# Kernel tuning notes

Hardware: AMD Instinct MI355X
Metric: run time of the kernel (lower is better)

Reference implementation:

```python
import jax, jax.numpy as jnp
import numpy as np

B, DIM, MID, H, W = 4, 256, 128, 128, 128
EPS = 1e-5


def _conv(x, w, pad):
    # x: [B,C,H,W], w: [O,I,k,k]
    return jax.lax.conv_general_dilated(
        x, w, window_strides=(1, 1), padding=[(pad, pad), (pad, pad)],
        dimension_numbers=('NCHW', 'OIHW', 'NCHW'))


def _bn(x, g, b, m, v):
    inv = jax.lax.rsqrt(v + EPS)
    scale = (g * inv)[None, :, None, None]
    shift = (b - m * g * inv)[None, :, None, None]
    return x * scale + shift


def _convbnrelu(x, w, g, b, m, v):
    return jax.nn.relu(_bn(_conv(x, w, 1), g, b, m, v))


# CornerNet directional pools: sequential max-accumulation scans.
def top_pool(x):     # max over y' >= y  -> reversed cummax along H
    return jax.lax.cummax(x, axis=2, reverse=True)

def bottom_pool(x):  # max over y' <= y
    return jax.lax.cummax(x, axis=2)

def left_pool(x):    # max over x' >= x
    return jax.lax.cummax(x, axis=3, reverse=True)

def right_pool(x):   # max over x' <= x
    return jax.lax.cummax(x, axis=3)


def setup_inputs() -> dict:
    key = jax.random.key(0)
    ks = jax.random.split(key, 32)
    it = iter(ks)

    def w(shape, scale=0.05):
        return jax.random.normal(next(it), shape, jnp.float32) * scale

    def bn_params(c):
        return (jnp.ones((c,), jnp.float32) + 0.1 * jax.random.normal(next(it), (c,), jnp.float32),
                0.1 * jax.random.normal(next(it), (c,), jnp.float32),
                0.1 * jax.random.normal(next(it), (c,), jnp.float32),
                jax.random.uniform(next(it), (c,), jnp.float32) + 0.5)

    inp = {'x': jax.random.normal(next(it), (B, DIM, H, W), jnp.float32)}

    inp['p1_w'] = w((MID, DIM, 3, 3))
    inp['p1_g'], inp['p1_b'], inp['p1_m'], inp['p1_v'] = bn_params(MID)
    inp['p2_w'] = w((MID, DIM, 3, 3))
    inp['p2_g'], inp['p2_b'], inp['p2_m'], inp['p2_v'] = bn_params(MID)
    inp['p_w'] = w((DIM, MID, 3, 3))
    inp['p_g'], inp['p_b'], inp['p_m'], inp['p_v'] = bn_params(DIM)
    inp['c1_w'] = w((DIM, DIM, 1, 1))
    inp['c1_g'], inp['c1_b'], inp['c1_m'], inp['c1_v'] = bn_params(DIM)
    inp['c2_w'] = w((DIM, DIM, 3, 3))
    inp['c2_g'], inp['c2_b'], inp['c2_m'], inp['c2_v'] = bn_params(DIM)
    return inp


def reference(x,
              p1_w, p1_g, p1_b, p1_m, p1_v,
              p2_w, p2_g, p2_b, p2_m, p2_v,
              p_w, p_g, p_b, p_m, p_v,
              c1_w, c1_g, c1_b, c1_m, c1_v,
              c2_w, c2_g, c2_b, c2_m, c2_v):
    # branch 1: conv-bn-relu -> top pool -> bottom pool
    pool1 = bottom_pool(top_pool(_convbnrelu(x, p1_w, p1_g, p1_b, p1_m, p1_v)))
    # branch 2: conv-bn-relu -> left pool -> right pool
    pool2 = right_pool(left_pool(_convbnrelu(x, p2_w, p2_g, p2_b, p2_m, p2_v)))
    # merge branch
    p_bn1 = _bn(_conv(pool1 + pool2, p_w, 1), p_g, p_b, p_m, p_v)
    # skip branch: 1x1 conv + bn
    bn1 = _bn(_conv(x, c1_w, 0), c1_g, c1_b, c1_m, c1_v)
    # residual add + relu, then final conv-bn-relu
    return _convbnrelu(jax.nn.relu(p_bn1 + bn1), c2_w, c2_g, c2_b, c2_m, c2_v)
```

## Files before the change

kernel.cpp:

```cpp
#include <hip/hip_runtime.h>
#include <hip/hip_bf16.h>
#include <math.h>


constexpr int NB   = 4;
constexpr int CDIM = 256;
constexpr int CMID = 128;
constexpr int HS   = 128;
constexpr int WS   = 128;
constexpr float EPS = 1e-5f;

typedef __bf16 bf16x8 __attribute__((ext_vector_type(8)));
typedef float  f32x4  __attribute__((ext_vector_type(4)));

#define AS1 __attribute__((address_space(1)))
#define AS3 __attribute__((address_space(3)))

__device__ __forceinline__ void load16_lds(const void* gsrc, void* ldst) {
    __builtin_amdgcn_global_load_lds((const AS1 unsigned int*)gsrc,
                                     (AS3 unsigned int*)ldst, 16, 0, 0);
}

__global__ __launch_bounds__(512) void k_xprep(const float* __restrict__ xin,
                                               __hip_bfloat16* __restrict__ Xc)
{
    const int y = blockIdx.x;
    const int b = blockIdx.y;
    const int t = threadIdx.x;
    __shared__ __hip_bfloat16 lds[128 * 264];
#pragma unroll
    for (int k = 0; k < 16; ++k) {
        int idx = t + k * 512;
        int ci = idx >> 5, x4 = idx & 31;
        f32x4 v = *(const f32x4*)(xin + (((size_t)b * CDIM + ci) * HS + y) * WS + x4 * 4);
#pragma unroll
        for (int j = 0; j < 4; ++j)
            lds[(x4 * 4 + j) * 264 + ci] = __float2bfloat16(v[j]);
    }
    __syncthreads();
#pragma unroll
    for (int k = 0; k < 8; ++k) {
        int i = t + k * 512;
        int x = i >> 5, c8 = i & 31;
        bf16x8 vv = *(const bf16x8*)(lds + x * 264 + c8 * 8);
        *(bf16x8*)(Xc + ((size_t)(b * 128 + y) * 128 + x) * 256 + c8 * 8) = vv;
    }
}

__global__ __launch_bounds__(256) void k_wprep_all(
    const float* __restrict__ p1w, const float* __restrict__ p2w,
    const float* __restrict__ c2w, const float* __restrict__ c1w,
    __hip_bfloat16* __restrict__ Aw1, __hip_bfloat16* __restrict__ Aw2,
    __hip_bfloat16* __restrict__ Aw5, __hip_bfloat16* __restrict__ Aw4,
    f32x4* __restrict__ zdst)
{
    const int bid = blockIdx.x;
    const int t   = threadIdx.x;
    if (bid < 512) {
        const float* W; __hip_bfloat16* A; int co;
        if (bid < 128)      { W = p1w; A = Aw1; co = bid; }
        else if (bid < 256) { W = p2w; A = Aw2; co = bid - 128; }
        else                { W = c2w; A = Aw5; co = bid - 256; }
#pragma unroll
        for (int tap = 0; tap < 9; ++tap)
            A[(size_t)co * 2304 + tap * 256 + t] =
                __float2bfloat16(W[((size_t)co * CDIM + t) * 9 + tap]);
    } else if (bid < 640) {
        int base = (bid - 512) * 512 + t;
        Aw4[base]       = __float2bfloat16(c1w[base]);
        Aw4[base + 256] = __float2bfloat16(c1w[base + 256]);
    } else if (bid < 768) {
        zdst[(size_t)(bid - 640) * 256 + t] = (f32x4){0.f, 0.f, 0.f, 0.f};
    } else {
        if (t < 16) zdst[32768 + t] = (f32x4){0.f, 0.f, 0.f, 0.f};
    }
}

template<int MODE>
__global__ __launch_bounds__(512, 2) void k_conv3(
    const __hip_bfloat16* __restrict__ Xc,
    const __hip_bfloat16* __restrict__ AwA, const __hip_bfloat16* __restrict__ AwB,
    const float* __restrict__ zbuf,
    const float* __restrict__ g1, const float* __restrict__ b1,
    const float* __restrict__ m1, const float* __restrict__ v1,
    const float* __restrict__ g2, const float* __restrict__ b2,
    const float* __restrict__ m2, const float* __restrict__ v2,
    float* __restrict__ out0, unsigned* __restrict__ cmax,
    unsigned* __restrict__ rmax, int CO)
{
    const int y0     = blockIdx.x * 4;
    const int branch = blockIdx.y;
    const int b      = blockIdx.z;
    const int co0    = (MODE == 0) ? branch * 128 : 0;

    const __hip_bfloat16* Aw = (MODE == 1 && branch) ? AwB : AwA;
    const float* gg  = (MODE == 1 && branch) ? g2 : g1;
    const float* bbp = (MODE == 1 && branch) ? b2 : b1;
    const float* mmp = (MODE == 1 && branch) ? m2 : m1;
    const float* vvp = (MODE == 1 && branch) ? v2 : v1;

    constexpr int BUFB = 896 * 64;
    __shared__ alignas(16) char smb[2 * BUFB];
    __shared__ float s_sc[128], s_sh[128];
    __shared__ unsigned s_red[4][128];

    const int t    = threadIdx.x;
    const int lane = t & 63;
    const int w    = t >> 6;
    const int ml   = lane & 15;
    const int q    = lane >> 4;
    const int yy    = w >> 1;
    const int mbase = (w & 1) * 64;

    const int cc  = (t & 3) ^ ((t >> 3) & 3);
    const int col = t >> 2;

    if (t < 128) {
        int co = co0 + t;
        float iv = rsqrtf(vvp[co] + EPS);
        float sc = gg[co] * iv;
        s_sc[t] = sc;
        s_sh[t] = bbp[co] - mmp[co] * sc;
    }
    if (MODE == 1 && branch == 1) ((unsigned*)s_red)[t] = 0u;

    f32x4 acc[4][8];
#pragma unroll
    for (int mt = 0; mt < 4; ++mt)
#pragma unroll
        for (int nt = 0; nt < 8; ++nt)
            acc[mt][nt] = (f32x4){0.f, 0.f, 0.f, 0.f};

    const __hip_bfloat16* bbase = Xc + (size_t)(b * 128) * 128 * 256;
    const char* zrow = (const char*)zbuf + cc * 16;

    auto stage_A = [&](char* dst, int p, int nky, int ncih) {
        const __hip_bfloat16* src = Aw + (size_t)(co0 + col) * 2304
            + (3 * nky + p) * 256 + ncih * 32 + cc * 8;
        load16_lds(src, dst + (size_t)(t + p * 512) * 16);
    };
    auto stage_B = [&](char* dst, int p, int nky, int ncih) {
        const int gy = y0 + nky - 1 + (p - 3);
        const __hip_bfloat16* src = ((unsigned)gy < 128u)
            ? bbase + ((size_t)(gy * 128 + col)) * 256 + ncih * 32 + cc * 8
            : (const __hip_bfloat16*)zrow;
        load16_lds(src, dst + (size_t)(t + p * 512) * 16);
    };

    bf16x8 BZERO;
#pragma unroll
    for (int k = 0; k < 8; ++k) BZERO[k] = (__bf16)0.0f;

    stage_B(smb, 3, 0, 0); stage_B(smb, 4, 0, 0); stage_B(smb, 5, 0, 0);
    stage_B(smb, 6, 0, 0);
    stage_A(smb, 0, 0, 0); stage_A(smb, 1, 0, 0); stage_A(smb, 2, 0, 0);

#define WAITB(N) \
    asm volatile("s_waitcnt vmcnt(" #N ")" ::: "memory"); \
    __builtin_amdgcn_s_barrier(); \
    __builtin_amdgcn_sched_barrier(0);

#define DS_PHASE(J, CB) \
    bf16x8 af[4], bfv[8]; \
    { \
        _Pragma("unroll") \
        for (int mt = 0; mt < 4; ++mt) { \
            const int ra = (J) * 128 + mbase + mt * 16 + ml; \
            const int sa = q ^ ((ra >> 1) & 3); \
            af[mt] = *(const bf16x8*)((CB) + (size_t)ra * 64 + sa * 16); \
        } \
        _Pragma("unroll") \
        for (int nt = 0; nt < 8; ++nt) { \
            const int rbl = nt * 16 + ml + (J) - 1; \
            const int rbc = rbl < 0 ? 0 : (rbl > 127 ? 127 : rbl); \
            const int rb  = 384 + yy * 128 + rbc; \
            const int sb  = q ^ ((rb >> 1) & 3); \
            bf16x8 bv = *(const bf16x8*)((CB) + (size_t)rb * 64 + sb * 16); \
            bfv[nt] = ((unsigned)rbl < 128u) ? bv : BZERO; \
        } \
    }

#define MFMA_PHASE() \
    __builtin_amdgcn_s_setprio(1); \
    _Pragma("unroll") \
    for (int mt = 0; mt < 4; ++mt) \
        _Pragma("unroll") \
        for (int nt = 0; nt < 8; ++nt) \
            acc[mt][nt] = __builtin_amdgcn_mfma_f32_16x16x32_bf16( \
                af[mt], bfv[nt], acc[mt][nt], 0, 0, 0); \
    __builtin_amdgcn_s_setprio(0);

#pragma unroll 1
    for (int step = 0; step < 23; ++step) {
        const char* cb_ = smb + (size_t)(step & 1) * BUFB;
        char*       nb_ = smb + (size_t)((step + 1) & 1) * BUFB;
        const int nstep = step + 1;
        const int nky = nstep >> 3, ncih = nstep & 7;
        {
            WAITB(2)
            DS_PHASE(0, cb_)
            stage_B(nb_, 3, nky, ncih);
            stage_B(nb_, 4, nky, ncih);
            stage_B(nb_, 5, nky, ncih);
            MFMA_PHASE()
        }
        {
            WAITB(4)
            DS_PHASE(1, cb_)
            stage_B(nb_, 6, nky, ncih);
            stage_A(nb_, 0, nky, ncih);
            MFMA_PHASE()
        }
        {
            WAITB(5)
            DS_PHASE(2, cb_)
            stage_A(nb_, 1, nky, ncih);
            stage_A(nb_, 2, nky, ncih);
            MFMA_PHASE()
        }
    }
    {
        const char* cb_ = smb + BUFB;
        { WAITB(2) DS_PHASE(0, cb_) MFMA_PHASE() }
        { WAITB(1) DS_PHASE(1, cb_) MFMA_PHASE() }
        { WAITB(0) DS_PHASE(2, cb_) MFMA_PHASE() }
    }
#undef WAITB
#undef DS_PHASE
#undef MFMA_PHASE

    if (MODE == 1 && branch == 0) {
        unsigned* colred = (unsigned*)smb;
#pragma unroll
        for (int k2 = 0; k2 < 32; ++k2) colred[t + k2 * 512] = 0u;
        __syncthreads();
    }

#pragma unroll
    for (int mt = 0; mt < 4; ++mt) {
#pragma unroll
        for (int r = 0; r < 4; ++r) {
            const int cl = mbase + mt * 16 + q * 4 + r;
            const float sc = s_sc[cl], sh = s_sh[cl];
            const int co = co0 + cl;
            unsigned rmx = 0u;
#pragma unroll
            for (int nt = 0; nt < 8; ++nt) {
                float va = fmaxf(acc[mt][nt][r] * sc + sh, 0.f);
                const int x = nt * 16 + ml;
                if (MODE == 0) {
                    out0[(((size_t)b * CO + co) * HS + y0 + yy) * WS + x] = va;
                } else if (branch == 0) {
                    atomicMax(((unsigned*)smb) + cl * 128 + x, __float_as_uint(va));
                } else {
                    rmx = max(rmx, __float_as_uint(va));
                }
            }
            if (MODE == 1 && branch == 1) atomicMax(&s_red[yy][cl], rmx);
        }
    }

    if (MODE == 1) {
        __syncthreads();
        if (branch == 0) {
            unsigned* colred = (unsigned*)smb;
#pragma unroll
            for (int k2 = 0; k2 < 32; ++k2) {
                int idx = t + k2 * 512;
                atomicMax(cmax + ((size_t)(b * 128 + (idx >> 7))) * 128 + (idx & 127),
                          colred[idx]);
            }
        } else {
            atomicMax(rmax + ((size_t)(b * 128 + (t & 127))) * 128 + y0 + (t >> 7),
                      s_red[t >> 7][t & 127]);
        }
    }
}

__global__ __launch_bounds__(128) void k_uv(
    const float* __restrict__ pw, const float* __restrict__ cm,
    const float* __restrict__ rm,
    __hip_bfloat16* __restrict__ U, __hip_bfloat16* __restrict__ V)
{
    const int co   = blockIdx.x;
    const int b    = blockIdx.y;
    const int mode = blockIdx.z;
    const int p    = threadIdx.x;
    float acc0 = 0.f, acc1 = 0.f, acc2 = 0.f;
    const float* base = (mode == 0) ? cm : rm;
    for (int ci = 0; ci < CMID; ++ci) {
        const float* w9 = pw + (co * CMID + ci) * 9;
        float s0[3], s1[3], s2[3];
        if (mode == 0) {
#pragma unroll
            for (int k = 0; k < 3; ++k) {
                float a = w9[k], qq = w9[3 + k], r = w9[6 + k];
                s0[k] = qq + r; s1[k] = a + qq + r; s2[k] = a + qq;
            }
        } else {
#pragma unroll
            for (int k = 0; k < 3; ++k) {
                float a = w9[k*3 + 0], qq = w9[k*3 + 1], r = w9[k*3 + 2];
                s0[k] = qq + r; s1[k] = a + qq + r; s2[k] = a + qq;
            }
        }
        const float* v = base + (b * CMID + ci) * 128;
#pragma unroll
        for (int k = 0; k < 3; ++k) {
            int pos = p + k - 1;
            if ((unsigned)pos < 128u) {
                float vv = v[pos];
                acc0 += s0[k] * vv; acc1 += s1[k] * vv; acc2 += s2[k] * vv;
            }
        }
    }
    __hip_bfloat16* dst = (mode == 0) ? U : V;
    dst[((0 * NB + b) * CDIM + co) * 128 + p] = __float2bfloat16(acc0);
    dst[((1 * NB + b) * CDIM + co) * 128 + p] = __float2bfloat16(acc1);
    dst[((2 * NB + b) * CDIM + co) * 128 + p] = __float2bfloat16(acc2);
}

__global__ __launch_bounds__(256, 2) void k_merge_mfma(
    const __hip_bfloat16* __restrict__ Xc, const __hip_bfloat16* __restrict__ Aw4,
    const __hip_bfloat16* __restrict__ U, const __hip_bfloat16* __restrict__ V,
    const float* __restrict__ pg, const float* __restrict__ pb,
    const float* __restrict__ pm, const float* __restrict__ pv,
    const float* __restrict__ cg, const float* __restrict__ cb,
    const float* __restrict__ cmn, const float* __restrict__ cv,
    __hip_bfloat16* __restrict__ Rc)
{
    const int y = blockIdx.x;
    const int b = blockIdx.y;
    __shared__ __hip_bfloat16 smem[32768];
    __shared__ float s_psc[256], s_psh[256], s_csc[256], s_csh[256];
    __shared__ float s_v0[256], s_vm[256], s_v1[256];
    char* smb = (char*)smem;
    const int t = threadIdx.x, lane = t & 63, w = t >> 6;
    const int ml = lane & 15, q = lane >> 4;
    const int mbase = w * 64;
    const int yc = (y == 0) ? 0 : ((y == HS - 1) ? 2 : 1);

    {
        int co = t;
        float iv = rsqrtf(pv[co] + EPS);
        float psc = pg[co] * iv;
        s_psc[co] = psc;
        s_psh[co] = pb[co] - pm[co] * psc;
        float iv2 = rsqrtf(cv[co] + EPS);
        float csc = cg[co] * iv2;
        s_csc[co] = csc;
        s_csh[co] = cb[co] - cmn[co] * csc;
        const size_t vb = ((size_t)b * CDIM + co) * 128 + y;
        const size_t cstr = (size_t)NB * CDIM * 128;
        s_v0[co] = __bfloat162float(V[vb]);
        s_vm[co] = __bfloat162float(V[cstr + vb]);
        s_v1[co] = __bfloat162float(V[2 * cstr + vb]);
    }

    f32x4 acc[4][8];
#pragma unroll
    for (int mt = 0; mt < 4; ++mt)
#pragma unroll
        for (int nt = 0; nt < 8; ++nt)
            acc[mt][nt] = (f32x4){0.f, 0.f, 0.f, 0.f};

    const __hip_bfloat16* brow = Xc + (size_t)(b * 128 + y) * 128 * 256;
#pragma unroll 1
    for (int ks = 0; ks < 4; ++ks) {
#pragma unroll
        for (int p = 0; p < 12; ++p) {
            int i   = t + p * 256;
            int row = i >> 3, sl = i & 7;
            int c   = sl ^ (row & 7);
            const __hip_bfloat16* src = (row < 256)
                ? Aw4 + (size_t)row * 256 + ks * 64 + c * 8
                : brow + (size_t)(row - 256) * 256 + ks * 64 + c * 8;
            load16_lds(src, smb + (size_t)i * 16);
        }
        __syncthreads();
#pragma unroll
        for (int s = 0; s < 2; ++s) {
            bf16x8 af[4], bfv[8];
#pragma unroll
            for (int mt = 0; mt < 4; ++mt) {
                const int ra = mbase + mt * 16 + ml;
                const int coff = ((s * 4 + q) ^ (ra & 7)) * 16;
                af[mt] = *(const bf16x8*)(smb + (size_t)ra * 128 + coff);
            }
#pragma unroll
            for (int nt = 0; nt < 8; ++nt) {
                const int rb = 256 + nt * 16 + ml;
                const int coff = ((s * 4 + q) ^ (rb & 7)) * 16;
                bfv[nt] = *(const bf16x8*)(smb + (size_t)rb * 128 + coff);
            }
#pragma unroll
            for (int mt = 0; mt < 4; ++mt)
#pragma unroll
                for (int nt = 0; nt < 8; ++nt)
                    acc[mt][nt] = __builtin_amdgcn_mfma_f32_16x16x32_bf16(
                        af[mt], bfv[nt], acc[mt][nt], 0, 0, 0);
        }
        __syncthreads();
    }

    const __hip_bfloat16* Ub = U + ((size_t)(yc * NB + b) * CDIM + mbase) * 128;
#pragma unroll
    for (int k = 0; k < 16; ++k) {
        int i = lane + k * 64;
        load16_lds(Ub + (size_t)i * 8, smb + (size_t)w * 16384 + (size_t)i * 16);
    }
    __syncthreads();
    const __hip_bfloat16* ulds = smem + w * 8192;

#pragma unroll
    for (int mt = 0; mt < 4; ++mt) {
#pragma unroll
        for (int nt = 0; nt < 8; ++nt) {
            const int x = nt * 16 + ml;
            unsigned long long pk = 0;
#pragma unroll
            for (int r = 0; r < 4; ++r) {
                const int cl = mt * 16 + q * 4 + r;
                const int co = mbase + cl;
                float u  = __bfloat162float(ulds[cl * 128 + x]);
                float vt = (x == 0) ? s_v0[co] : ((x == WS - 1) ? s_v1[co] : s_vm[co]);
                float val = fmaxf((u + vt) * s_psc[co] + s_psh[co]
                                  + acc[mt][nt][r] * s_csc[co] + s_csh[co], 0.f);
                __hip_bfloat16 hb = __float2bfloat16(val);
                unsigned short bits;
                __builtin_memcpy(&bits, &hb, 2);
                pk |= (unsigned long long)bits << (16 * r);
            }
            *(unsigned long long*)((char*)Rc +
                ((size_t)((b * 128 + y) * 128 + x) * 256 + mbase + mt * 16 + q * 4) * 2) = pk;
        }
    }
}

extern "C" void kernel_launch(void* const* d_in, const int* in_sizes, int n_in,
                              void* d_out, int out_size, void* d_ws, size_t ws_size,
                              hipStream_t stream)
{
    (void)in_sizes; (void)n_in; (void)out_size; (void)ws_size;
    const float* x    = (const float*)d_in[0];
    const float* p1_w = (const float*)d_in[1];
    const float* p1_g = (const float*)d_in[2];
    const float* p1_b = (const float*)d_in[3];
    const float* p1_m = (const float*)d_in[4];
    const float* p1_v = (const float*)d_in[5];
    const float* p2_w = (const float*)d_in[6];
    const float* p2_g = (const float*)d_in[7];
    const float* p2_b = (const float*)d_in[8];
    const float* p2_m = (const float*)d_in[9];
    const float* p2_v = (const float*)d_in[10];
    const float* p_w  = (const float*)d_in[11];
    const float* p_g  = (const float*)d_in[12];
    const float* p_b  = (const float*)d_in[13];
    const float* p_m  = (const float*)d_in[14];
    const float* p_v  = (const float*)d_in[15];
    const float* c1_w = (const float*)d_in[16];
    const float* c1_g = (const float*)d_in[17];
    const float* c1_b = (const float*)d_in[18];
    const float* c1_m = (const float*)d_in[19];
    const float* c1_v = (const float*)d_in[20];
    const float* c2_w = (const float*)d_in[21];
    const float* c2_g = (const float*)d_in[22];
    const float* c2_b = (const float*)d_in[23];
    const float* c2_m = (const float*)d_in[24];
    const float* c2_v = (const float*)d_in[25];
    float* out = (float*)d_out;
    char* ws = (char*)d_ws;

    __hip_bfloat16* Xc   = (__hip_bfloat16*)ws;
    __hip_bfloat16* Rc   = (__hip_bfloat16*)(ws + 33554432);
    __hip_bfloat16* Ubuf = (__hip_bfloat16*)(ws + 67108864);
    __hip_bfloat16* Vbuf = (__hip_bfloat16*)(ws + 67895296);
    __hip_bfloat16* Aw1  = (__hip_bfloat16*)(ws + 67108864);
    __hip_bfloat16* Aw2  = (__hip_bfloat16*)(ws + 67698688);
    __hip_bfloat16* Aw5  = (__hip_bfloat16*)(ws + 68681728);
    __hip_bfloat16* Aw4  = (__hip_bfloat16*)(ws + 69861376);
    unsigned*       cmaxU = (unsigned*)(ws + 69992448);
    unsigned*       rmaxU = (unsigned*)(ws + 70254592);
    float*          zbuf  = (float*)(ws + 70516736);

    k_wprep_all<<<dim3(769), 256, 0, stream>>>(
        p1_w, p2_w, c2_w, c1_w, Aw1, Aw2, Aw5, Aw4, (f32x4*)(ws + 69992448));
    k_xprep<<<dim3(128, 4), 512, 0, stream>>>(x, Xc);

    k_conv3<1><<<dim3(32, 2, 4), 512, 0, stream>>>(
        Xc, Aw1, Aw2, zbuf,
        p1_g, p1_b, p1_m, p1_v, p2_g, p2_b, p2_m, p2_v,
        nullptr, cmaxU, rmaxU, CMID);

    k_uv<<<dim3(256, 4, 2), 128, 0, stream>>>(
        p_w, (const float*)cmaxU, (const float*)rmaxU, Ubuf, Vbuf);

    k_merge_mfma<<<dim3(128, 4), 256, 0, stream>>>(
        Xc, Aw4, Ubuf, Vbuf, p_g, p_b, p_m, p_v,
        c1_g, c1_b, c1_m, c1_v, Rc);

    k_conv3<0><<<dim3(32, 2, 4), 512, 0, stream>>>(
        Rc, Aw5, nullptr, zbuf,
        c2_g, c2_b, c2_m, c2_v, nullptr, nullptr, nullptr, nullptr,
        out, nullptr, nullptr, CDIM);
}
```

Measured before the change: 388.3 us.

## Replace three-phase staggered pipeline with one barrier per step and prefetched fragments

Swaps the per-ky-phase schedule, which used three partial vmcnt waits and barriers per K step, for a single full wait and barrier per step. All seven global-to-LDS loads for the next buffer are issued up front, and LDS fragment reads for the three ky phases are interleaved with MFMA clusters (read 0, read 1, mma 0, read 2, mma 1, mma 2). The loop now covers the final step itself instead of using a separate epilogue, and the s_setprio hints are dropped. This cuts barrier count but waits for every global load before any compute starts, which may expose load latency. It also raises register pressure from holding three fragment sets.

```diff
diff --git a/kernel.cpp b/kernel.cpp
--- a/kernel.cpp
+++ b/kernel.cpp
@@ -151,23 +151,13 @@
 #pragma unroll
     for (int k = 0; k < 8; ++k) BZERO[k] = (__bf16)0.0f;
 
-    stage_B(smb, 3, 0, 0); stage_B(smb, 4, 0, 0); stage_B(smb, 5, 0, 0);
-    stage_B(smb, 6, 0, 0);
-    stage_A(smb, 0, 0, 0); stage_A(smb, 1, 0, 0); stage_A(smb, 2, 0, 0);
-
-#define WAITB(N) \
-    asm volatile("s_waitcnt vmcnt(" #N ")" ::: "memory"); \
-    __builtin_amdgcn_s_barrier(); \
-    __builtin_amdgcn_sched_barrier(0);
-
-#define DS_PHASE(J, CB) \
-    bf16x8 af[4], bfv[8]; \
+#define READF(J, CB, AF, BF) \
     { \
         _Pragma("unroll") \
         for (int mt = 0; mt < 4; ++mt) { \
             const int ra = (J) * 128 + mbase + mt * 16 + ml; \
             const int sa = q ^ ((ra >> 1) & 3); \
-            af[mt] = *(const bf16x8*)((CB) + (size_t)ra * 64 + sa * 16); \
+            AF[mt] = *(const bf16x8*)((CB) + (size_t)ra * 64 + sa * 16); \
         } \
         _Pragma("unroll") \
         for (int nt = 0; nt < 8; ++nt) { \
@@ -176,60 +166,55 @@
             const int rb  = 384 + yy * 128 + rbc; \
             const int sb  = q ^ ((rb >> 1) & 3); \
             bf16x8 bv = *(const bf16x8*)((CB) + (size_t)rb * 64 + sb * 16); \
-            bfv[nt] = ((unsigned)rbl < 128u) ? bv : BZERO; \
+            BF[nt] = ((unsigned)rbl < 128u) ? bv : BZERO; \
         } \
     }
 
-#define MFMA_PHASE() \
-    __builtin_amdgcn_s_setprio(1); \
+#define MFMA_CL(AF, BF) \
     _Pragma("unroll") \
     for (int mt = 0; mt < 4; ++mt) \
         _Pragma("unroll") \
         for (int nt = 0; nt < 8; ++nt) \
             acc[mt][nt] = __builtin_amdgcn_mfma_f32_16x16x32_bf16( \
-                af[mt], bfv[nt], acc[mt][nt], 0, 0, 0); \
-    __builtin_amdgcn_s_setprio(0);
+                AF[mt], BF[nt], acc[mt][nt], 0, 0, 0);
+
+    stage_B(smb, 3, 0, 0); stage_B(smb, 4, 0, 0); stage_B(smb, 5, 0, 0);
+    stage_B(smb, 6, 0, 0);
+    stage_A(smb, 0, 0, 0); stage_A(smb, 1, 0, 0); stage_A(smb, 2, 0, 0);
 
 #pragma unroll 1
-    for (int step = 0; step < 23; ++step) {
+    for (int step = 0; step < 24; ++step) {
         const char* cb_ = smb + (size_t)(step & 1) * BUFB;
         char*       nb_ = smb + (size_t)((step + 1) & 1) * BUFB;
         const int nstep = step + 1;
         const int nky = nstep >> 3, ncih = nstep & 7;
-        {
-            WAITB(2)
-            DS_PHASE(0, cb_)
+
+        asm volatile("s_waitcnt vmcnt(0)" ::: "memory");
+        __builtin_amdgcn_s_barrier();
+
+        if (step < 23) {
             stage_B(nb_, 3, nky, ncih);
             stage_B(nb_, 4, nky, ncih);
             stage_B(nb_, 5, nky, ncih);
-            MFMA_PHASE()
-        }
-        {
-            WAITB(4)
-            DS_PHASE(1, cb_)
             stage_B(nb_, 6, nky, ncih);
             stage_A(nb_, 0, nky, ncih);
-            MFMA_PHASE()
-        }
-        {
-            WAITB(5)
-            DS_PHASE(2, cb_)
             stage_A(nb_, 1, nky, ncih);
             stage_A(nb_, 2, nky, ncih);
-            MFMA_PHASE()
-        }
-    }
-    {
-        const char* cb_ = smb + BUFB;
-        { WAITB(2) DS_PHASE(0, cb_) MFMA_PHASE() }
-        { WAITB(1) DS_PHASE(1, cb_) MFMA_PHASE() }
-        { WAITB(0) DS_PHASE(2, cb_) MFMA_PHASE() }
-    }
-#undef WAITB
-#undef DS_PHASE
-#undef MFMA_PHASE
+        }
+
+        bf16x8 a0[4], b0[8], a1[4], b1[8], a2[4], b2[8];
+        READF(0, cb_, a0, b0)
+        READF(1, cb_, a1, b1)
+        MFMA_CL(a0, b0)
+        READF(2, cb_, a2, b2)
+        MFMA_CL(a1, b1)
+        MFMA_CL(a2, b2)
+    }
+#undef READF
+#undef MFMA_CL
 
     if (MODE == 1 && branch == 0) {
+        __syncthreads();
         unsigned* colred = (unsigned*)smb;
 #pragma unroll
         for (int k2 = 0; k2 < 32; ++k2) colred[t + k2 * 512] = 0u;
```

New measurement: 407.9 us. +5.0%, slower.
